# Optimization experiments

Hardware: AMD Instinct MI355X
Metric: run time of the kernel (lower is better)

## Reference

```python
import jax, jax.numpy as jnp
import numpy as np

DIM = 2048
HEADS = 16
HEAD_DIM = DIM // HEADS
EPS = 1e-5


def layernorm(x, g, b):
    mu = jnp.mean(x, axis=-1, keepdims=True)
    var = jnp.mean(jnp.square(x - mu), axis=-1, keepdims=True)
    return (x - mu) * jax.lax.rsqrt(var + EPS) * g + b


def bitlinear(x, w):
    # BitNet b1.58: per-tensor ternary weight quant + per-token int8 absmax activation quant
    ws = jnp.clip(jnp.mean(jnp.abs(w)), 1e-5, None)          # weight scale (mean |w|)
    wq = jnp.clip(jnp.round(w / ws), -1.0, 1.0) * ws          # ternary {-1,0,1}*ws
    xs = 127.0 / jnp.clip(jnp.max(jnp.abs(x), axis=-1, keepdims=True), 1e-5, None)
    xq = jnp.clip(jnp.round(x * xs), -128.0, 127.0) / xs      # int8 absmax, dequantized
    return jnp.einsum('bnc,oc->bno', xq, wq)


def attention(x, w_qkv, w_proj):
    B, N, C = x.shape
    qkv = bitlinear(x, w_qkv).reshape(B, N, 3, HEADS, HEAD_DIM)
    q, k, v = [qkv[:, :, i].transpose(0, 2, 1, 3) for i in range(3)]  # [B,H,N,D]
    scores = jnp.einsum('bhqd,bhkd->bhqk', q, k) / jnp.sqrt(jnp.asarray(HEAD_DIM, x.dtype))
    attn = jax.nn.softmax(scores, axis=-1)
    o = jnp.einsum('bhqk,bhkd->bhqd', attn, v)
    o = o.transpose(0, 2, 1, 3).reshape(B, N, C)
    return bitlinear(o, w_proj)


def setup_inputs() -> dict:
    key = jax.random.key(0)
    ks = jax.random.split(key, 9)
    s = 0.02
    return {
        'x': jax.random.normal(ks[0], (2, 2048, DIM), dtype=jnp.float32),
        'w_qkv': jax.random.normal(ks[1], (3 * DIM, DIM), dtype=jnp.float32) * s,
        'w_proj': jax.random.normal(ks[2], (DIM, DIM), dtype=jnp.float32) * s,
        'w_fc1': jax.random.normal(ks[3], (4 * DIM, DIM), dtype=jnp.float32) * s,
        'w_fc2': jax.random.normal(ks[4], (DIM, 4 * DIM), dtype=jnp.float32) * s,
        'g1': jnp.ones((DIM,), jnp.float32),
        'b1': jnp.zeros((DIM,), jnp.float32),
        'g2': jnp.ones((DIM,), jnp.float32),
        'b2': jnp.zeros((DIM,), jnp.float32),
    }


def reference(x, w_qkv, w_proj, w_fc1, w_fc2, g1, b1, g2, b2):
    x = x + attention(layernorm(x, g1, b1), w_qkv, w_proj)
    h = bitlinear(layernorm(x, g2, b2), w_fc1)
    h = jax.nn.gelu(h, approximate=False)
    h = bitlinear(h, w_fc2)
    return x + h
```

## Files before the change

kernel.cpp:

```cpp
#include <hip/hip_runtime.h>
#include <cstdint>

#define DEVI __device__ __forceinline__

typedef int v4i __attribute__((ext_vector_type(4)));
typedef short v8s __attribute__((ext_vector_type(8)));
typedef float v4f __attribute__((ext_vector_type(4)));

DEVI float bf_lo(unsigned u) { return __uint_as_float(u << 16); }
DEVI float bf_hi(unsigned u) { return __uint_as_float(u & 0xffff0000u); }
DEVI float bf2f(unsigned short h) { return __uint_as_float(((unsigned)h) << 16); }
DEVI unsigned short f2bf(float f) {
  unsigned u = __float_as_uint(f);
  u += 0x7fffu + ((u >> 16) & 1u);
  return (unsigned short)(u >> 16);
}

DEVI void async_copy16(void* l, const void* g) {
  __builtin_amdgcn_global_load_lds((const __attribute__((address_space(1))) void*)g,
                                   (__attribute__((address_space(3))) void*)l,
                                   16, 0, 0);
}

DEVI float wave_sum(float v) {
#pragma unroll
  for (int o = 32; o > 0; o >>= 1) v += __shfl_xor(v, o, 64);
  return v;
}
DEVI float wave_max(float v) {
#pragma unroll
  for (int o = 32; o > 0; o >>= 1) v = fmaxf(v, __shfl_xor(v, o, 64));
  return v;
}

__global__ __launch_bounds__(256) void absum_kernel(const float* __restrict__ w, long n,
                                                    float* __restrict__ acc) {
  long stride = (long)gridDim.x * 1024;
  float s = 0.f;
  for (long i = ((long)blockIdx.x * 256 + threadIdx.x) * 4; i < n; i += stride) {
    float4 v = *(const float4*)(w + i);
    s += fabsf(v.x) + fabsf(v.y) + fabsf(v.z) + fabsf(v.w);
  }
  s = wave_sum(s);
  __shared__ float sc[4];
  int tid = threadIdx.x;
  if ((tid & 63) == 0) sc[tid >> 6] = s;
  __syncthreads();
  if (tid == 0) atomicAdd(acc, sc[0] + sc[1] + sc[2] + sc[3]);
}

__global__ __launch_bounds__(256) void wquant_kernel(const float* __restrict__ w, long n4,
                                                     const float* __restrict__ acc, float cnt,
                                                     signed char* __restrict__ out, int kshift) {
  float wsv = fmaxf(acc[0] / cnt, 1e-5f);
  float inv = 1.0f / wsv;
  int K = 1 << kshift;
  long stride = (long)gridDim.x * 256;
  for (long i = (long)blockIdx.x * 256 + threadIdx.x; i < n4; i += stride) {
    float4 v = *(const float4*)(w + i * 4);
    int q0 = max(-1, min(1, (int)rintf(v.x * inv)));
    int q1 = max(-1, min(1, (int)rintf(v.y * inv)));
    int q2 = max(-1, min(1, (int)rintf(v.z * inv)));
    int q3 = max(-1, min(1, (int)rintf(v.w * inv)));
    unsigned r = (q0 & 0xff) | ((q1 & 0xff) << 8) | ((q2 & 0xff) << 16) | ((q3 & 0xff) << 24);
    long flat = i * 4;
    int n = (int)(flat >> kshift);
    int k = (int)(flat & (K - 1));
    long off = ((long)(n >> 4) * (K >> 6) + (k >> 6)) * 1024 +
               (((k >> 4) & 3) * 16 + (n & 15)) * 16 + (k & 15);
    *(unsigned*)(out + off) = r;
  }
}

__global__ __launch_bounds__(256) void ln_quant_kernel(const float* __restrict__ x,
                                                       const float* __restrict__ g,
                                                       const float* __restrict__ b,
                                                       signed char* __restrict__ q,
                                                       float* __restrict__ inv_s) {
  int row = blockIdx.x, tid = threadIdx.x;
  const float4* xr = (const float4*)(x + (long)row * 2048);
  float4 a0 = xr[tid * 2], a1 = xr[tid * 2 + 1];
  float xv[8] = {a0.x, a0.y, a0.z, a0.w, a1.x, a1.y, a1.z, a1.w};
  float s = 0.f, s2 = 0.f;
#pragma unroll
  for (int e = 0; e < 8; ++e) { s += xv[e]; s2 += xv[e] * xv[e]; }
  s = wave_sum(s); s2 = wave_sum(s2);
  __shared__ float sc[8];
  if ((tid & 63) == 0) { sc[tid >> 6] = s; sc[4 + (tid >> 6)] = s2; }
  __syncthreads();
  float mean = (sc[0] + sc[1] + sc[2] + sc[3]) * (1.f / 2048.f);
  float var = (sc[4] + sc[5] + sc[6] + sc[7]) * (1.f / 2048.f) - mean * mean;
  float rs = 1.0f / sqrtf(var + 1e-5f);
  float4 g0 = ((const float4*)g)[tid * 2], g1v = ((const float4*)g)[tid * 2 + 1];
  float4 b0 = ((const float4*)b)[tid * 2], b1v = ((const float4*)b)[tid * 2 + 1];
  float gv[8] = {g0.x, g0.y, g0.z, g0.w, g1v.x, g1v.y, g1v.z, g1v.w};
  float bv[8] = {b0.x, b0.y, b0.z, b0.w, b1v.x, b1v.y, b1v.z, b1v.w};
  float y[8];
  float am = 0.f;
#pragma unroll
  for (int e = 0; e < 8; ++e) {
    y[e] = (xv[e] - mean) * rs * gv[e] + bv[e];
    am = fmaxf(am, fabsf(y[e]));
  }
  am = wave_max(am);
  __syncthreads();
  if ((tid & 63) == 0) sc[tid >> 6] = am;
  __syncthreads();
  am = fmaxf(fmaxf(sc[0], sc[1]), fmaxf(sc[2], sc[3]));
  float c = fmaxf(am, 1e-5f);
  float xs = 127.0f / c;
  union { signed char c8[8]; int2 v; } u;
#pragma unroll
  for (int e = 0; e < 8; ++e) {
    int t = (int)rintf(y[e] * xs);
    u.c8[e] = (signed char)max(-128, min(127, t));
  }
  ((int2*)(q + (long)row * 2048))[tid] = u.v;
  if (tid == 0) inv_s[row] = c * (1.0f / 127.0f);
}

template <int R>
__global__ __launch_bounds__(256) void row_quant_kernel(const unsigned short* __restrict__ in,
                                                        signed char* __restrict__ q,
                                                        float* __restrict__ inv_s) {
  constexpr int V = R / 2048;
  int row = blockIdx.x, tid = threadIdx.x;
  const uint4* p = (const uint4*)(in + (long)row * R);
  float y[V * 8];
  float am = 0.f;
#pragma unroll
  for (int v = 0; v < V; ++v) {
    uint4 d = p[tid * V + v];
    unsigned xw[4] = {d.x, d.y, d.z, d.w};
#pragma unroll
    for (int k = 0; k < 4; ++k) {
      y[v * 8 + k * 2] = bf_lo(xw[k]);
      y[v * 8 + k * 2 + 1] = bf_hi(xw[k]);
    }
  }
#pragma unroll
  for (int e = 0; e < V * 8; ++e) am = fmaxf(am, fabsf(y[e]));
  am = wave_max(am);
  __shared__ float sc[4];
  if ((tid & 63) == 0) sc[tid >> 6] = am;
  __syncthreads();
  am = fmaxf(fmaxf(sc[0], sc[1]), fmaxf(sc[2], sc[3]));
  float c = fmaxf(am, 1e-5f);
  float xs = 127.0f / c;
  signed char* qr = q + (long)row * R;
#pragma unroll
  for (int v = 0; v < V; ++v) {
    union { signed char c8[8]; long l; } u;
#pragma unroll
    for (int k = 0; k < 8; ++k) {
      int t = (int)rintf(y[v * 8 + k] * xs);
      u.c8[k] = (signed char)max(-128, min(127, t));
    }
    ((long*)qr)[tid * V + v] = u.l;
  }
  if (tid == 0) inv_s[row] = c * (1.0f / 127.0f);
}

template <int EPI>
__global__ __launch_bounds__(256)
void gemm_i8(const signed char* __restrict__ A, const signed char* __restrict__ Bp,
             int N, int K, const float* __restrict__ wacc, float wcount,
             const float* __restrict__ inv_s, const float* __restrict__ res,
             void* __restrict__ outp) {
  __shared__ signed char As[2][128 * 128];
  int tid = threadIdx.x;
  int idx = blockIdx.x;
  int r8 = idx & 7, rest = idx >> 3;
  int mb = rest & 31;
  int nb = (rest >> 5) * 8 + r8;
  int m0 = mb * 128, n0 = nb * 128;
  int w = tid >> 6, lane = tid & 63;
  int wm = (w >> 1) * 64, wn = (w & 1) * 64;
  int lr = lane & 15, q = lane >> 4;

  v4i acc[4][4] = {};

  int srow = w * 32 + (lane >> 3);
  int scol = (lane & 7) ^ ((lane >> 3) & 7);
  const signed char* ga = A + (long)(m0 + srow) * K + scol * 16;

  int nkb = K >> 7;
  const signed char* gbp[4];
#pragma unroll
  for (int t = 0; t < 4; ++t) {
    int ntile = (n0 >> 4) + (w & 1) * 4 + t;
    gbp[t] = Bp + (long)ntile * (K >> 6) * 1024 + lane * 16;
  }

  v4i bf_cur[2][4], bf_nxt[2][4];
#pragma unroll
  for (int i = 0; i < 4; ++i)
    async_copy16(&As[0][(w * 256 + i * 64) * 16], ga + i * 8 * K);
#pragma unroll
  for (int s = 0; s < 2; ++s)
#pragma unroll
    for (int t = 0; t < 4; ++t) bf_cur[s][t] = *(const v4i*)(gbp[t] + s * 1024);
  __syncthreads();

  int buf = 0;
  for (int kb = 0; kb < nkb; ++kb) {
    if (kb + 1 < nkb) {
#pragma unroll
      for (int i = 0; i < 4; ++i)
        async_copy16(&As[buf ^ 1][(w * 256 + i * 64) * 16], ga + i * 8 * K + (kb + 1) * 128);
#pragma unroll
      for (int s = 0; s < 2; ++s)
#pragma unroll
        for (int t = 0; t < 4; ++t)
          bf_nxt[s][t] = *(const v4i*)(gbp[t] + ((kb + 1) * 2 + s) * 1024);
    }
#pragma unroll
    for (int s = 0; s < 2; ++s) {
      v4i af[4];
#pragma unroll
      for (int i = 0; i < 4; ++i) {
        int row = wm + i * 16 + lr;
        af[i] = *(const v4i*)(&As[buf][(row * 8 + ((s * 4 + q) ^ (lr & 7))) * 16]);
      }
#pragma unroll
      for (int i = 0; i < 4; ++i)
#pragma unroll
        for (int j = 0; j < 4; ++j)
          acc[i][j] = __builtin_amdgcn_mfma_i32_16x16x64_i8(af[i], bf_cur[s][j], acc[i][j], 0, 0, 0);
    }
    __syncthreads();
    if (kb + 1 < nkb) {
#pragma unroll
      for (int s = 0; s < 2; ++s)
#pragma unroll
        for (int t = 0; t < 4; ++t) bf_cur[s][t] = bf_nxt[s][t];
    }
    buf ^= 1;
  }

  float wsv = fmaxf(wacc[0] / wcount, 1e-5f);
#pragma unroll
  for (int i = 0; i < 4; ++i) {
    int rowbase = m0 + wm + i * 16 + (lane >> 4) * 4;
#pragma unroll
    for (int r = 0; r < 4; ++r) {
      int row = rowbase + r;
      float s = wsv * inv_s[row];
#pragma unroll
      for (int j = 0; j < 4; ++j) {
        int col = n0 + wn + j * 16 + (lane & 15);
        long off = (long)row * N + col;
        float v = (float)acc[i][j][r] * s;
        if constexpr (EPI == 0) {
          ((unsigned short*)outp)[off] = f2bf(v);
        } else if constexpr (EPI == 1) {
          ((float*)outp)[off] = v + res[off];
        } else {
          float gvv = 0.5f * v * (1.0f + erff(v * 0.70710678118654752f));
          ((unsigned short*)outp)[off] = f2bf(gvv);
        }
      }
    }
  }
}

#define GIB_PHASE(RB, BFC, VMISSUE, WAITSTR, TAIL)                                      \
  {                                                                                     \
    v4i af[4];                                                                          \
    _Pragma("unroll") for (int j = 0; j < 4; ++j) {                                     \
      int m = 2 * p + (j >> 1), kc = j & 1;                                             \
      int row = wm + m * 16 + lr;                                                       \
      af[j] = *(const v4i*)(&As[(RB)][(row * 8 + ((kc * 4 + q) ^ (lr & 7))) * 16]);     \
    }                                                                                   \
    __builtin_amdgcn_sched_barrier(0);                                                  \
    VMISSUE                                                                             \
    __builtin_amdgcn_sched_barrier(0);                                                  \
    __builtin_amdgcn_s_barrier();                                                       \
    asm volatile(WAITSTR ::: "memory");                                                 \
    __builtin_amdgcn_sched_barrier(0);                                                  \
    __builtin_amdgcn_s_setprio(1);                                                      \
    _Pragma("unroll") for (int j = 0; j < 2; ++j)                                       \
      _Pragma("unroll") for (int t = 0; t < 4; ++t)                                     \
        _Pragma("unroll") for (int kc = 0; kc < 2; ++kc)                                \
          acc[2 * p + j][t] = __builtin_amdgcn_mfma_i32_16x16x64_i8(                    \
              af[j * 2 + kc], BFC[kc][t], acc[2 * p + j][t], 0, 0, 0);                  \
    __builtin_amdgcn_s_setprio(0);                                                      \
    __builtin_amdgcn_sched_barrier(0);                                                  \
    TAIL                                                                                \
    __builtin_amdgcn_s_barrier();                                                       \
  }

#define GIB_STAGE(RBD)                                                                  \
  _Pragma("unroll") for (int i = 0; i < 4; ++i)                                         \
    async_copy16(&As[(RBD)][(w * 256 + i * 64) * 16],                                   \
                 ga + (long)i * 8 * K + (kb + 1) * 128);

#define GIB_LOADB(DST, HALF)                                                            \
  _Pragma("unroll") for (int t = 0; t < 4; ++t)                                         \
    asm volatile("global_load_dwordx4 %0, %1, off"                                      \
                 : "=v"(DST[HALF][t])                                                   \
                 : "v"(gbp[t] + (long)((kb + 1) * 2 + (HALF)) * 1024)                   \
                 : "memory");

#define GIB_VMTAIL                                                                      \
  asm volatile("s_waitcnt vmcnt(8)" ::: "memory");                                      \
  __builtin_amdgcn_sched_barrier(0);

#define GIB_ITER_MAIN(RB, BFC, BFN)                                                     \
  {                                                                                     \
    { constexpr int p = 0;                                                              \
      GIB_PHASE(RB, BFC, GIB_STAGE((RB) ^ 1), "s_waitcnt vmcnt(4) lgkmcnt(0)", ) }      \
    { constexpr int p = 1;                                                              \
      GIB_PHASE(RB, BFC, GIB_LOADB(BFN, 0), "s_waitcnt lgkmcnt(0)", ) }                 \
    { constexpr int p = 2;                                                              \
      GIB_PHASE(RB, BFC, GIB_LOADB(BFN, 1), "s_waitcnt lgkmcnt(0)", ) }                 \
    { constexpr int p = 3;                                                              \
      GIB_PHASE(RB, BFC, , "s_waitcnt lgkmcnt(0)", GIB_VMTAIL) }                        \
  }

#define GIB_ITER_LAST(RB, BFC)                                                          \
  {                                                                                     \
    { constexpr int p = 0;                                                              \
      GIB_PHASE(RB, BFC, , "s_waitcnt vmcnt(0) lgkmcnt(0)", ) }                         \
    { constexpr int p = 1;                                                              \
      GIB_PHASE(RB, BFC, , "s_waitcnt lgkmcnt(0)", ) }                                  \
    { constexpr int p = 2;                                                              \
      GIB_PHASE(RB, BFC, , "s_waitcnt lgkmcnt(0)", ) }                                  \
    { constexpr int p = 3;                                                              \
      GIB_PHASE(RB, BFC, , "s_waitcnt lgkmcnt(0)", ) }                                  \
  }

template <int EPI>
__global__ __launch_bounds__(512, 2)
void gemm_i8_big(const signed char* __restrict__ A, const signed char* __restrict__ Bp,
                 int N, int K, const float* __restrict__ wacc, float wcount,
                 const float* __restrict__ inv_s, const float* __restrict__ res,
                 void* __restrict__ outp) {
  __shared__ signed char As[2][256 * 128];
  int tid = threadIdx.x;
  int idx = blockIdx.x;
  int r8 = idx & 7, rest = idx >> 3;
  int mb = rest & 15;
  int nb = (rest >> 4) * 8 + r8;
  int m0 = mb * 256, n0 = nb * 256;
  int w = tid >> 6, lane = tid & 63;
  int wm = (w >> 2) * 128, wn = (w & 3) * 64;
  int lr = lane & 15, q = lane >> 4;

  v4i acc[8][4] = {};

  int srow = w * 32 + (lane >> 3);
  int scol = (lane & 7) ^ ((lane >> 3) & 7);
  const signed char* ga = A + (long)(m0 + srow) * K + scol * 16;

  int nkt = K >> 7;
  const signed char* gbp[4];
#pragma unroll
  for (int t = 0; t < 4; ++t) {
    int ntile = ((n0 + wn) >> 4) + t;
    gbp[t] = Bp + (long)ntile * (K >> 6) * 1024 + lane * 16;
  }

  v4i bfA[2][4], bfB[2][4];
#pragma unroll
  for (int i = 0; i < 4; ++i)
    async_copy16(&As[0][(w * 256 + i * 64) * 16], ga + (long)i * 8 * K);
  __builtin_amdgcn_sched_barrier(0);
#pragma unroll
  for (int s = 0; s < 2; ++s)
#pragma unroll
    for (int t = 0; t < 4; ++t)
      asm volatile("global_load_dwordx4 %0, %1, off"
                   : "=v"(bfA[s][t]) : "v"(gbp[t] + (long)s * 1024) : "memory");
  __builtin_amdgcn_sched_barrier(0);
  asm volatile("s_waitcnt vmcnt(8)" ::: "memory");
  __builtin_amdgcn_sched_barrier(0);
  __builtin_amdgcn_s_barrier();

  for (int kb2 = 0; kb2 < nkt - 2; kb2 += 2) {
    { int kb = kb2;     GIB_ITER_MAIN(0, bfA, bfB) }
    { int kb = kb2 + 1; GIB_ITER_MAIN(1, bfB, bfA) }
  }
  { int kb = nkt - 2; GIB_ITER_MAIN(0, bfA, bfB) }
  GIB_ITER_LAST(1, bfB)

  float wsv = fmaxf(wacc[0] / wcount, 1e-5f);
#pragma unroll
  for (int m = 0; m < 8; ++m) {
    int rowbase = m0 + wm + m * 16 + q * 4;
#pragma unroll
    for (int r = 0; r < 4; ++r) {
      int row = rowbase + r;
      float s = wsv * inv_s[row];
#pragma unroll
      for (int j = 0; j < 4; ++j) {
        int col = n0 + wn + j * 16 + lr;
        long off = (long)row * N + col;
        float v = (float)acc[m][j][r] * s;
        if constexpr (EPI == 0) {
          ((unsigned short*)outp)[off] = f2bf(v);
        } else if constexpr (EPI == 1) {
          ((float*)outp)[off] = v + res[off];
        } else {
          float gvv = 0.5f * v * (1.0f + erff(v * 0.70710678118654752f));
          ((unsigned short*)outp)[off] = f2bf(gvv);
        }
      }
    }
  }
}

DEVI int sigma_k(int y) {
  return (y & 35) | (((y >> 3) & 1) << 4) | (((y >> 2) & 1) << 3) | (((y >> 4) & 1) << 2);
}

DEVI void stage_k(const unsigned short* kbase_g, int k0, char* ks, int w, int lane) {
#pragma unroll
  for (int i = 0; i < 2; ++i) {
    int c = i * 512 + w * 64 + lane;
    int key = c >> 4;
    int dch = (c & 15) ^ (key & 15);
    async_copy16(ks + (i * 512 + w * 64) * 16,
                 kbase_g + (long)(k0 + sigma_k(key)) * 6144 + dch * 8);
  }
}

DEVI void load_v(const unsigned short* vbase_g, int k0, int kg, int dg, uint2* lv) {
#pragma unroll
  for (int i = 0; i < 4; ++i)
    lv[i] = *(const uint2*)(vbase_g + (long)(k0 + kg * 4 + i) * 6144 + dg * 4);
}

DEVI void repack_v(const uint2* lv, unsigned short* vt, int kg, int dg) {
#pragma unroll
  for (int jd = 0; jd < 4; ++jd) {
    union { unsigned short s[4]; unsigned long long u; } pk;
#pragma unroll
    for (int i = 0; i < 4; ++i) {
      unsigned word = (jd < 2) ? lv[i].x : lv[i].y;
      pk.s[i] = (unsigned short)((jd & 1) ? (word >> 16) : (word & 0xffffu));
    }
    *(unsigned long long*)(vt + (dg * 4 + jd) * 72 + kg * 4) = pk.u;
  }
}

__global__ __launch_bounds__(512, 4)
void fattn_kernel(const unsigned short* __restrict__ qkv, unsigned short* __restrict__ out) {
  constexpr int VROW = 72;
  __shared__ __align__(16) char Ks[2][16384];
  __shared__ __align__(16) unsigned short Vt[2][128 * VROW];

  int tid = threadIdx.x;
  int w = tid >> 6, lane = tid & 63;
  int l = lane & 15, q = lane >> 4;
  int idx = blockIdx.x;
  int r8 = idx & 7, rest = idx >> 3;
  int qt = rest & 15;
  int bh = (rest >> 4) * 8 + r8;
  int bb = bh >> 4, hh = bh & 15;
  const unsigned short* base = qkv + (long)bb * 2048 * 6144;
  int q0 = qt * 128;

  v8s aq[4];
  {
    const unsigned short* qrow = base + (long)(q0 + w * 16 + l) * 6144 + hh * 128;
#pragma unroll
    for (int kf = 0; kf < 4; ++kf) aq[kf] = *(const v8s*)(qrow + kf * 32 + q * 8);
  }

  v4f oacc[8] = {};
  float mrow = -1e30f, lrow = 0.f;

  const unsigned short* kbase_g = base + 2048 + hh * 128;
  const unsigned short* vbase_g = base + 4096 + hh * 128;
  int kg = tid & 15, dg = tid >> 4;
  constexpr float SC = 0.08838834764831845f;

  stage_k(kbase_g, 0, Ks[0], w, lane);
  uint2 lv[4];
  load_v(vbase_g, 0, kg, dg, lv);
  repack_v(lv, Vt[0], kg, dg);
  __syncthreads();

  for (int kt = 0; kt < 32; ++kt) {
    const char* ksc = Ks[kt & 1];
    const unsigned short* vtc = Vt[kt & 1];
    bool more = kt < 31;
    if (more) {
      stage_k(kbase_g, (kt + 1) * 64, Ks[(kt + 1) & 1], w, lane);
      load_v(vbase_g, (kt + 1) * 64, kg, dg, lv);
    }

    v4f sacc[4] = {};
#pragma unroll
    for (int kf = 0; kf < 4; ++kf) {
#pragma unroll
      for (int t = 0; t < 4; ++t) {
        int ch = (t * 16 + l) * 16 + ((kf * 4 + q) ^ l);
        v8s bk = *(const v8s*)(ksc + ch * 16);
        sacc[t] = __builtin_amdgcn_mfma_f32_16x16x32_bf16(bk, aq[kf], sacc[t], 0, 0, 0);
      }
    }

    float rm = -1e30f;
#pragma unroll
    for (int t = 0; t < 4; ++t)
#pragma unroll
      for (int r = 0; r < 4; ++r) rm = fmaxf(rm, sacc[t][r]);
    rm *= SC;
    rm = fmaxf(rm, __shfl_xor(rm, 16, 64));
    rm = fmaxf(rm, __shfl_xor(rm, 32, 64));
    float mnew = fmaxf(mrow, rm);
    if (__any(mnew - mrow > 8.0f)) {
      float alpha = __expf(mrow - mnew);
      mrow = mnew;
      lrow *= alpha;
#pragma unroll
      for (int r = 0; r < 4; ++r) {
        float ao = __shfl(alpha, q * 4 + r, 64);
#pragma unroll
        for (int t = 0; t < 8; ++t) oacc[t][r] *= ao;
      }
    }
    float rs = 0.f;
#pragma unroll
    for (int t = 0; t < 4; ++t)
#pragma unroll
      for (int r = 0; r < 4; ++r) {
        float pv = __expf(fmaf(sacc[t][r], SC, -mrow));
        sacc[t][r] = pv;
        rs += pv;
      }
    rs += __shfl_xor(rs, 16, 64);
    rs += __shfl_xor(rs, 32, 64);
    lrow += rs;

    union { unsigned u[4]; v8s s; } pa[2];
#pragma unroll
    for (int s2 = 0; s2 < 2; ++s2)
#pragma unroll
      for (int j2 = 0; j2 < 4; ++j2) {
        int tt = s2 * 2 + (j2 >> 1);
        int r0 = (j2 & 1) * 2;
        unsigned wrd;
        asm("v_cvt_pk_bf16_f32 %0, %1, %2"
            : "=v"(wrd) : "v"(sacc[tt][r0]), "v"(sacc[tt][r0 + 1]));
        pa[s2].u[j2] = wrd;
      }

#pragma unroll
    for (int s2 = 0; s2 < 2; ++s2) {
#pragma unroll
      for (int t = 0; t < 8; ++t) {
        v8s bv = *(const v8s*)(vtc + (t * 16 + l) * VROW + s2 * 32 + q * 8);
        oacc[t] = __builtin_amdgcn_mfma_f32_16x16x32_bf16(pa[s2].s, bv, oacc[t], 0, 0, 0);
      }
    }

    if (more) repack_v(lv, Vt[(kt + 1) & 1], kg, dg);
    __syncthreads();
  }

#pragma unroll
  for (int r = 0; r < 4; ++r) {
    float lr = __shfl(lrow, q * 4 + r, 64);
    float inv = 1.0f / lr;
    long grow = (long)bb * 2048 + q0 + w * 16 + q * 4 + r;
    unsigned short* orow = out + grow * 2048 + hh * 128;
#pragma unroll
    for (int t = 0; t < 8; ++t) orow[t * 16 + l] = f2bf(oacc[t][r] * inv);
  }
}

extern "C" void kernel_launch(void* const* d_in, const int* in_sizes, int n_in,
                              void* d_out, int out_size, void* d_ws, size_t ws_size,
                              hipStream_t stream) {
  (void)in_sizes; (void)n_in; (void)out_size; (void)ws_size;
  const float* x      = (const float*)d_in[0];
  const float* w_qkv  = (const float*)d_in[1];
  const float* w_proj = (const float*)d_in[2];
  const float* w_fc1  = (const float*)d_in[3];
  const float* w_fc2  = (const float*)d_in[4];
  const float* g1 = (const float*)d_in[5];
  const float* b1 = (const float*)d_in[6];
  const float* g2 = (const float*)d_in[7];
  const float* b2 = (const float*)d_in[8];

  char* wsb = (char*)d_ws;
  float* acc = (float*)wsb;
  size_t off = 256;
  signed char* q8 = (signed char*)(wsb + off);       off += (size_t)4096 * 8192;
  float* invs = (float*)(wsb + off);                 off += 16384;
  signed char* wq_qkv = (signed char*)(wsb + off);   off += (size_t)6144 * 2048;
  signed char* wq_proj = (signed char*)(wsb + off);  off += (size_t)2048 * 2048;
  signed char* wq_fc1 = (signed char*)(wsb + off);   off += (size_t)8192 * 2048;
  signed char* wq_fc2 = (signed char*)(wsb + off);   off += (size_t)2048 * 8192;
  unsigned short* qkvh = (unsigned short*)(wsb + off); off += (size_t)4096 * 8192 * 2;
  unsigned short* obuf = (unsigned short*)(wsb + off); off += (size_t)4096 * 2048 * 2;
  float* x2 = (float*)(wsb + off);                   off += (size_t)4096 * 2048 * 4;

  hipMemsetAsync(acc, 0, 256, stream);

  absum_kernel<<<dim3(1024), 256, 0, stream>>>(w_qkv, (long)6144 * 2048, acc + 0);
  absum_kernel<<<dim3(512),  256, 0, stream>>>(w_proj, (long)2048 * 2048, acc + 1);
  absum_kernel<<<dim3(1024), 256, 0, stream>>>(w_fc1, (long)8192 * 2048, acc + 2);
  absum_kernel<<<dim3(1024), 256, 0, stream>>>(w_fc2, (long)2048 * 8192, acc + 3);

  wquant_kernel<<<dim3(1024), 256, 0, stream>>>(w_qkv, (long)6144 * 2048 / 4, acc + 0, 12582912.f, wq_qkv, 11);
  wquant_kernel<<<dim3(1024), 256, 0, stream>>>(w_proj, (long)2048 * 2048 / 4, acc + 1, 4194304.f, wq_proj, 11);
  wquant_kernel<<<dim3(1024), 256, 0, stream>>>(w_fc1, (long)8192 * 2048 / 4, acc + 2, 16777216.f, wq_fc1, 11);
  wquant_kernel<<<dim3(1024), 256, 0, stream>>>(w_fc2, (long)2048 * 8192 / 4, acc + 3, 16777216.f, wq_fc2, 13);

  ln_quant_kernel<<<4096, 256, 0, stream>>>(x, g1, b1, q8, invs);
  gemm_i8_big<0><<<16 * 24, 512, 0, stream>>>(q8, wq_qkv, 6144, 2048, acc + 0, 12582912.f, invs, nullptr, qkvh);
  fattn_kernel<<<512, 512, 0, stream>>>(qkvh, obuf);
  row_quant_kernel<2048><<<4096, 256, 0, stream>>>(obuf, q8, invs);
  gemm_i8<1><<<16 * 32, 256, 0, stream>>>(q8, wq_proj, 2048, 2048, acc + 1, 4194304.f, invs, x, x2);
  ln_quant_kernel<<<4096, 256, 0, stream>>>(x2, g2, b2, q8, invs);
  gemm_i8_big<2><<<16 * 32, 512, 0, stream>>>(q8, wq_fc1, 8192, 2048, acc + 2, 16777216.f, invs, nullptr, qkvh);
  row_quant_kernel<8192><<<4096, 256, 0, stream>>>(qkvh, q8, invs);
  gemm_i8<1><<<16 * 32, 256, 0, stream>>>(q8, wq_fc2, 2048, 8192, acc + 3, 16777216.f, invs, x2, (float*)d_out);
}
```

Baseline: 766.1 us.

## Batch weight quant launches and software-pipeline LDS fragment loads in big int8 GEMM

The four absum launches and four weight-quant launches become one launch each, with the weight picked by blockIdx&3, to cut launch overhead and tail idle time. In the big int8 GEMM, A-fragment LDS reads now use two register buffers (afA/afB) so the next phase's ds_reads are issued before the current phase's MFMAs, with lgkmcnt(4) partial waits instead of full drains. This hides LDS latency behind compute at the cost of more VGPRs, which could hurt occupancy or cause spills.

After: 763.9 us. About the same (-0.3%).

```diff
diff --git a/kernel.cpp b/kernel.cpp
--- a/kernel.cpp
+++ b/kernel.cpp
@@ -33,11 +33,19 @@
   return v;
 }
 
-__global__ __launch_bounds__(256) void absum_kernel(const float* __restrict__ w, long n,
-                                                    float* __restrict__ acc) {
-  long stride = (long)gridDim.x * 1024;
+__global__ __launch_bounds__(256) void absum4_kernel(const float* __restrict__ w0,
+                                                     const float* __restrict__ w1,
+                                                     const float* __restrict__ w2,
+                                                     const float* __restrict__ w3,
+                                                     float* __restrict__ acc) {
+  int t = blockIdx.x & 3;
+  int bid = blockIdx.x >> 2;
+  int nb = gridDim.x >> 2;
+  const float* w = t == 0 ? w0 : t == 1 ? w1 : t == 2 ? w2 : w3;
+  long n = t == 0 ? 12582912L : t == 1 ? 4194304L : 16777216L;
+  long stride = (long)nb * 1024;
   float s = 0.f;
-  for (long i = ((long)blockIdx.x * 256 + threadIdx.x) * 4; i < n; i += stride) {
+  for (long i = ((long)bid * 256 + threadIdx.x) * 4; i < n; i += stride) {
     float4 v = *(const float4*)(w + i);
     s += fabsf(v.x) + fabsf(v.y) + fabsf(v.z) + fabsf(v.w);
   }
@@ -46,17 +54,35 @@
   int tid = threadIdx.x;
   if ((tid & 63) == 0) sc[tid >> 6] = s;
   __syncthreads();
-  if (tid == 0) atomicAdd(acc, sc[0] + sc[1] + sc[2] + sc[3]);
-}
-
-__global__ __launch_bounds__(256) void wquant_kernel(const float* __restrict__ w, long n4,
-                                                     const float* __restrict__ acc, float cnt,
-                                                     signed char* __restrict__ out, int kshift) {
-  float wsv = fmaxf(acc[0] / cnt, 1e-5f);
+  if (tid == 0) atomicAdd(acc + t, sc[0] + sc[1] + sc[2] + sc[3]);
+}
+
+__global__ __launch_bounds__(256) void wquant4_kernel(const float* __restrict__ w0,
+                                                      const float* __restrict__ w1,
+                                                      const float* __restrict__ w2,
+                                                      const float* __restrict__ w3,
+                                                      const float* __restrict__ acc,
+                                                      signed char* __restrict__ o0,
+                                                      signed char* __restrict__ o1,
+                                                      signed char* __restrict__ o2,
+                                                      signed char* __restrict__ o3) {
+  int t = blockIdx.x & 3;
+  int bid = blockIdx.x >> 2;
+  int nb = gridDim.x >> 2;
+  const float* w;
+  signed char* out;
+  long n4;
+  float cnt;
+  int kshift;
+  if (t == 0)      { w = w0; out = o0; n4 = 3145728L; cnt = 12582912.f; kshift = 11; }
+  else if (t == 1) { w = w1; out = o1; n4 = 1048576L; cnt = 4194304.f;  kshift = 11; }
+  else if (t == 2) { w = w2; out = o2; n4 = 4194304L; cnt = 16777216.f; kshift = 11; }
+  else             { w = w3; out = o3; n4 = 4194304L; cnt = 16777216.f; kshift = 13; }
+  float wsv = fmaxf(acc[t] / cnt, 1e-5f);
   float inv = 1.0f / wsv;
   int K = 1 << kshift;
-  long stride = (long)gridDim.x * 256;
-  for (long i = (long)blockIdx.x * 256 + threadIdx.x; i < n4; i += stride) {
+  long stride = (long)nb * 256;
+  for (long i = (long)bid * 256 + threadIdx.x; i < n4; i += stride) {
     float4 v = *(const float4*)(w + i * 4);
     int q0 = max(-1, min(1, (int)rintf(v.x * inv)));
     int q1 = max(-1, min(1, (int)rintf(v.y * inv)));
@@ -264,14 +290,23 @@
   }
 }
 
-#define GIB_PHASE(RB, BFC, VMISSUE, WAITSTR, TAIL)                                      \
+#define GIB_DS(AF, MLO, RBUF)                                                           \
+  _Pragma("unroll") for (int j = 0; j < 4; ++j) {                                       \
+    int m = (MLO) + (j >> 1), kc = j & 1;                                               \
+    int row = wm + m * 16 + lr;                                                         \
+    AF[j] = *(const v4i*)(&As[(RBUF)][(row * 8 + ((kc * 4 + q) ^ (lr & 7))) * 16]);     \
+  }
+
+#define GIB_MM(AF, MLO, BFC)                                                            \
+  _Pragma("unroll") for (int j2 = 0; j2 < 2; ++j2)                                      \
+    _Pragma("unroll") for (int t = 0; t < 4; ++t)                                       \
+      _Pragma("unroll") for (int kc = 0; kc < 2; ++kc)                                  \
+        acc[(MLO) + j2][t] = __builtin_amdgcn_mfma_i32_16x16x64_i8(                     \
+            AF[j2 * 2 + kc], BFC[kc][t], acc[(MLO) + j2][t], 0, 0, 0);
+
+#define GIB_PH(DSISSUE, VMISSUE, WAITSTR, MMPART, TAIL)                                 \
   {                                                                                     \
-    v4i af[4];                                                                          \
-    _Pragma("unroll") for (int j = 0; j < 4; ++j) {                                     \
-      int m = 2 * p + (j >> 1), kc = j & 1;                                             \
-      int row = wm + m * 16 + lr;                                                       \
-      af[j] = *(const v4i*)(&As[(RB)][(row * 8 + ((kc * 4 + q) ^ (lr & 7))) * 16]);     \
-    }                                                                                   \
+    DSISSUE                                                                             \
     __builtin_amdgcn_sched_barrier(0);                                                  \
     VMISSUE                                                                             \
     __builtin_amdgcn_sched_barrier(0);                                                  \
@@ -279,11 +314,7 @@
     asm volatile(WAITSTR ::: "memory");                                                 \
     __builtin_amdgcn_sched_barrier(0);                                                  \
     __builtin_amdgcn_s_setprio(1);                                                      \
-    _Pragma("unroll") for (int j = 0; j < 2; ++j)                                       \
-      _Pragma("unroll") for (int t = 0; t < 4; ++t)                                     \
-        _Pragma("unroll") for (int kc = 0; kc < 2; ++kc)                                \
-          acc[2 * p + j][t] = __builtin_amdgcn_mfma_i32_16x16x64_i8(                    \
-              af[j * 2 + kc], BFC[kc][t], acc[2 * p + j][t], 0, 0, 0);                  \
+    MMPART                                                                              \
     __builtin_amdgcn_s_setprio(0);                                                      \
     __builtin_amdgcn_sched_barrier(0);                                                  \
     TAIL                                                                                \
@@ -308,26 +339,22 @@
 
 #define GIB_ITER_MAIN(RB, BFC, BFN)                                                     \
   {                                                                                     \
-    { constexpr int p = 0;                                                              \
-      GIB_PHASE(RB, BFC, GIB_STAGE((RB) ^ 1), "s_waitcnt vmcnt(4) lgkmcnt(0)", ) }      \
-    { constexpr int p = 1;                                                              \
-      GIB_PHASE(RB, BFC, GIB_LOADB(BFN, 0), "s_waitcnt lgkmcnt(0)", ) }                 \
-    { constexpr int p = 2;                                                              \
-      GIB_PHASE(RB, BFC, GIB_LOADB(BFN, 1), "s_waitcnt lgkmcnt(0)", ) }                 \
-    { constexpr int p = 3;                                                              \
-      GIB_PHASE(RB, BFC, , "s_waitcnt lgkmcnt(0)", GIB_VMTAIL) }                        \
+    GIB_PH(GIB_DS(afA, 0, RB) GIB_DS(afB, 2, RB), GIB_STAGE((RB) ^ 1),                  \
+           "s_waitcnt vmcnt(4) lgkmcnt(4)", GIB_MM(afA, 0, BFC), )                      \
+    GIB_PH(GIB_DS(afA, 4, RB), GIB_LOADB(BFN, 0),                                       \
+           "s_waitcnt lgkmcnt(4)", GIB_MM(afB, 2, BFC), )                               \
+    GIB_PH(GIB_DS(afB, 6, RB), GIB_LOADB(BFN, 1),                                       \
+           "s_waitcnt lgkmcnt(4)", GIB_MM(afA, 4, BFC), )                               \
+    GIB_PH(, , "s_waitcnt lgkmcnt(0)", GIB_MM(afB, 6, BFC), GIB_VMTAIL)                 \
   }
 
 #define GIB_ITER_LAST(RB, BFC)                                                          \
   {                                                                                     \
-    { constexpr int p = 0;                                                              \
-      GIB_PHASE(RB, BFC, , "s_waitcnt vmcnt(0) lgkmcnt(0)", ) }                         \
-    { constexpr int p = 1;                                                              \
-      GIB_PHASE(RB, BFC, , "s_waitcnt lgkmcnt(0)", ) }                                  \
-    { constexpr int p = 2;                                                              \
-      GIB_PHASE(RB, BFC, , "s_waitcnt lgkmcnt(0)", ) }                                  \
-    { constexpr int p = 3;                                                              \
-      GIB_PHASE(RB, BFC, , "s_waitcnt lgkmcnt(0)", ) }                                  \
+    GIB_PH(GIB_DS(afA, 0, RB) GIB_DS(afB, 2, RB), ,                                     \
+           "s_waitcnt vmcnt(0) lgkmcnt(4)", GIB_MM(afA, 0, BFC), )                      \
+    GIB_PH(GIB_DS(afA, 4, RB), , "s_waitcnt lgkmcnt(4)", GIB_MM(afB, 2, BFC), )         \
+    GIB_PH(GIB_DS(afB, 6, RB), , "s_waitcnt lgkmcnt(4)", GIB_MM(afA, 4, BFC), )         \
+    GIB_PH(, , "s_waitcnt lgkmcnt(0)", GIB_MM(afB, 6, BFC), )                           \
   }
 
 template <int EPI>
@@ -362,6 +389,7 @@
   }
 
   v4i bfA[2][4], bfB[2][4];
+  v4i afA[4], afB[4];
 #pragma unroll
   for (int i = 0; i < 4; ++i)
     async_copy16(&As[0][(w * 256 + i * 64) * 16], ga + (long)i * 8 * K);
@@ -601,15 +629,9 @@
 
   hipMemsetAsync(acc, 0, 256, stream);
 
-  absum_kernel<<<dim3(1024), 256, 0, stream>>>(w_qkv, (long)6144 * 2048, acc + 0);
-  absum_kernel<<<dim3(512),  256, 0, stream>>>(w_proj, (long)2048 * 2048, acc + 1);
-  absum_kernel<<<dim3(1024), 256, 0, stream>>>(w_fc1, (long)8192 * 2048, acc + 2);
-  absum_kernel<<<dim3(1024), 256, 0, stream>>>(w_fc2, (long)2048 * 8192, acc + 3);
-
-  wquant_kernel<<<dim3(1024), 256, 0, stream>>>(w_qkv, (long)6144 * 2048 / 4, acc + 0, 12582912.f, wq_qkv, 11);
-  wquant_kernel<<<dim3(1024), 256, 0, stream>>>(w_proj, (long)2048 * 2048 / 4, acc + 1, 4194304.f, wq_proj, 11);
-  wquant_kernel<<<dim3(1024), 256, 0, stream>>>(w_fc1, (long)8192 * 2048 / 4, acc + 2, 16777216.f, wq_fc1, 11);
-  wquant_kernel<<<dim3(1024), 256, 0, stream>>>(w_fc2, (long)2048 * 8192 / 4, acc + 3, 16777216.f, wq_fc2, 13);
+  absum4_kernel<<<4096, 256, 0, stream>>>(w_qkv, w_proj, w_fc1, w_fc2, acc);
+  wquant4_kernel<<<4096, 256, 0, stream>>>(w_qkv, w_proj, w_fc1, w_fc2, acc,
+                                           wq_qkv, wq_proj, wq_fc1, wq_fc2);
 
   ln_quant_kernel<<<4096, 256, 0, stream>>>(x, g1, b1, q8, invs);
   gemm_i8_big<0><<<16 * 24, 512, 0, stream>>>(q8, wq_qkv, 6144, 2048, acc + 0, 12582912.f, invs, nullptr, qkvh);
```
